# Performance work log

Measured on AMD Instinct MI355X. Metric: run time of the kernel, lower is better.

## Reference

```python
import jax, jax.numpy as jnp
import numpy as np

DIM = 1024
HEADS = 16
BIAS_INIT = 5.0
POST_LOG_SCALE = 1.0


def setup_inputs() -> dict:
    key = jax.random.key(0)
    kx, kw = jax.random.split(key)
    x = jax.random.normal(kx, (2, 2048, DIM), dtype=jnp.float32)
    # nn.Linear(dim, heads): weight [heads, dim], bias initialized to bias_init
    W = jax.random.normal(kw, (HEADS, DIM), dtype=jnp.float32) * (1.0 / np.sqrt(DIM))
    b = jnp.full((HEADS,), BIAS_INIT, dtype=jnp.float32)
    return {"x": x, "W": W, "b": b}


def reference(x, W, b):
    # linear -> [b, n, h], rearrange to [b, h, n], logsigmoid, scale
    logits = jnp.einsum('bnd,hd->bhn', x, W) + b[None, :, None]
    fg = jax.nn.log_sigmoid(logits) * POST_LOG_SCALE
    # cumulative sum over sequence
    fg = jnp.cumsum(fg, axis=-1)
    # pairwise subtract: bias[b,h,i,j] = fg[b,h,i] - fg[b,h,j] (causal case)
    return fg[:, :, :, None] - fg[:, :, None, :]
```

## Files before the change

### kernel.cpp

```cpp
#include <hip/hip_runtime.h>
#include <hip/hip_bf16.h>

#define DIM   1024
#define HEADS 16
#define B     2
#define N     2048
#define RPW   8

typedef float f32x4 __attribute__((ext_vector_type(4)));

__global__ __launch_bounds__(256) void logits_kernel(
    const float* __restrict__ x, const float* __restrict__ W,
    const float* __restrict__ bias, float* __restrict__ logits) {
  const int bn   = blockIdx.x;
  const int tid  = threadIdx.x;
  const int wave = tid >> 6;
  const int lane = tid & 63;

  const f32x4* xrow = (const f32x4*)(x + (size_t)bn * DIM);
  f32x4 xv[4];
#pragma unroll
  for (int k = 0; k < 4; ++k) xv[k] = xrow[lane * 4 + k];

#pragma unroll
  for (int hh = 0; hh < 4; ++hh) {
    const int h = wave * 4 + hh;
    const f32x4* wrow = (const f32x4*)(W + (size_t)h * DIM);
    float s = 0.0f;
#pragma unroll
    for (int k = 0; k < 4; ++k) {
      f32x4 wv = wrow[lane * 4 + k];
      s += wv.x * xv[k].x + wv.y * xv[k].y + wv.z * xv[k].z + wv.w * xv[k].w;
    }
#pragma unroll
    for (int off = 32; off > 0; off >>= 1) s += __shfl_down(s, off, 64);
    if (lane == 0) {
      const int b = bn >> 11;
      const int n = bn & (N - 1);
      logits[((size_t)(b * HEADS + h)) * N + n] = s + bias[h];
    }
  }
}

__device__ __forceinline__ float logsig(float z) {
  return fminf(z, 0.0f) - log1pf(__expf(-fabsf(z)));
}

__global__ __launch_bounds__(256) void cumsum_kernel(
    const float* __restrict__ logits, float* __restrict__ fg) {
  const int bh  = blockIdx.x;
  const int tid = threadIdx.x;
  const float* lp = logits + (size_t)bh * N;
  float*       fp = fg     + (size_t)bh * N;

  f32x4 a = ((const f32x4*)lp)[tid * 2];
  f32x4 c = ((const f32x4*)lp)[tid * 2 + 1];
  float v[8] = {a.x, a.y, a.z, a.w, c.x, c.y, c.z, c.w};

  float run = 0.0f;
#pragma unroll
  for (int i = 0; i < 8; ++i) { v[i] = logsig(v[i]); run += v[i]; v[i] = run; }
  const float total = run;

  const int lane = tid & 63, wv = tid >> 6;
  float sc = total;
#pragma unroll
  for (int off = 1; off < 64; off <<= 1) {
    float t = __shfl_up(sc, off, 64);
    if (lane >= off) sc += t;
  }

  __shared__ float wtot[4];
  if (lane == 63) wtot[wv] = sc;
  __syncthreads();
  float wofs = 0.0f;
  for (int w = 0; w < wv; ++w) wofs += wtot[w];

  const float base = wofs + sc - total;
  f32x4 o0 = {base + v[0], base + v[1], base + v[2], base + v[3]};
  f32x4 o1 = {base + v[4], base + v[5], base + v[6], base + v[7]};
  ((f32x4*)fp)[tid * 2]     = o0;
  ((f32x4*)fp)[tid * 2 + 1] = o1;
}

__global__ __launch_bounds__(256) void outer_kernel(
    const float* __restrict__ fg, float* __restrict__ out) {
  const int tid  = threadIdx.x;
  const int wave = tid >> 6;
  const int lane = tid & 63;
  const int gw   = blockIdx.x * 4 + wave;
  const int row0 = gw * RPW;
  const int bh   = row0 >> 11;
  const int i0   = row0 & (N - 1);

  const float* frow = fg + ((size_t)bh << 11);

  const f32x4* fj = (const f32x4*)frow;
  f32x4 vj[8];
#pragma unroll
  for (int k = 0; k < 8; ++k) vj[k] = fj[lane + k * 64];

  f32x4 fia = *(const f32x4*)(frow + i0);
  f32x4 fib = *(const f32x4*)(frow + i0 + 4);
  const float fi[RPW] = {fia.x, fia.y, fia.z, fia.w, fib.x, fib.y, fib.z, fib.w};

  f32x4* orow = (f32x4*)(out + ((size_t)row0 << 11));
#pragma unroll
  for (int r = 0; r < RPW; ++r) {
    const float f = fi[r];
#pragma unroll
    for (int k = 0; k < 8; ++k) {
      f32x4 v = vj[k];
      f32x4 s = {f - v.x, f - v.y, f - v.z, f - v.w};
      orow[lane + k * 64] = s;
    }
    orow += N / 4;
  }
}

extern "C" void kernel_launch(void* const* d_in, const int* in_sizes, int n_in,
                              void* d_out, int out_size, void* d_ws, size_t ws_size,
                              hipStream_t stream) {
  const float* x    = (const float*)d_in[0];
  const float* W    = (const float*)d_in[1];
  const float* bias = (const float*)d_in[2];
  float* out = (float*)d_out;

  float* logits = (float*)d_ws;
  float* fg     = logits + (size_t)B * HEADS * N;

  logits_kernel<<<B * N, 256, 0, stream>>>(x, W, bias, logits);
  cumsum_kernel<<<B * HEADS, 256, 0, stream>>>(logits, fg);
  outer_kernel<<<B * HEADS * N / (RPW * 4), 256, 0, stream>>>(fg, out);
}
```

Before: 123.4 us.

## Fuse logits, cumsum and outer-difference into one cooperative kernel with grid sync

Merges the three launches into a single cooperative persistent kernel that uses grid-wide syncs between the projection, the scan and the pairwise-difference phases. Each block processes four input rows in the projection phase and each wave writes sixteen output rows in the final phase. This is meant to remove inter-kernel launch gaps and tail effects. It adds grid barrier cost and depends on the grid being co-resident, falling back to separate kernels if the cooperative launch fails.

After: 334.8 us. +171.4%, slower.

```diff
diff --git a/kernel.cpp b/kernel.cpp
--- a/kernel.cpp
+++ b/kernel.cpp
@@ -1,13 +1,127 @@
 #include <hip/hip_runtime.h>
 #include <hip/hip_bf16.h>
+#include <hip/hip_cooperative_groups.h>
+
+namespace cg = cooperative_groups;
 
 #define DIM   1024
 #define HEADS 16
 #define B     2
 #define N     2048
-#define RPW   8
+#define BLOCKS 1024
 
 typedef float f32x4 __attribute__((ext_vector_type(4)));
+
+__device__ __forceinline__ float logsig(float z) {
+  return fminf(z, 0.0f) - log1pf(__expf(-fabsf(z)));
+}
+
+__global__ __launch_bounds__(256, 4) void fused_kernel(
+    const float* __restrict__ x, const float* __restrict__ W,
+    const float* __restrict__ bias, float* __restrict__ out,
+    float* __restrict__ logits, float* __restrict__ fg) {
+  cg::grid_group grid = cg::this_grid();
+  const int tid  = threadIdx.x;
+  const int wave = tid >> 6;
+  const int lane = tid & 63;
+
+  {
+    const int bn0 = blockIdx.x * 4;
+    for (int r = 0; r < 4; ++r) {
+      const int bn = bn0 + r;
+      const f32x4* xrow = (const f32x4*)(x + (size_t)bn * DIM);
+      f32x4 xv[4];
+#pragma unroll
+      for (int k = 0; k < 4; ++k) xv[k] = xrow[lane * 4 + k];
+#pragma unroll
+      for (int hh = 0; hh < 4; ++hh) {
+        const int h = wave * 4 + hh;
+        const f32x4* wrow = (const f32x4*)(W + (size_t)h * DIM);
+        float s = 0.0f;
+#pragma unroll
+        for (int k = 0; k < 4; ++k) {
+          f32x4 wv = wrow[lane * 4 + k];
+          s += wv.x * xv[k].x + wv.y * xv[k].y + wv.z * xv[k].z + wv.w * xv[k].w;
+        }
+#pragma unroll
+        for (int off = 32; off > 0; off >>= 1) s += __shfl_down(s, off, 64);
+        if (lane == 0) {
+          const int b = bn >> 11;
+          const int n = bn & (N - 1);
+          logits[((size_t)(b * HEADS + h)) * N + n] = s + bias[h];
+        }
+      }
+    }
+  }
+
+  grid.sync();
+
+  if (blockIdx.x < B * HEADS) {
+    const int bh = blockIdx.x;
+    const float* lp = logits + (size_t)bh * N;
+    float*       fp = fg     + (size_t)bh * N;
+
+    f32x4 a = ((const f32x4*)lp)[tid * 2];
+    f32x4 c = ((const f32x4*)lp)[tid * 2 + 1];
+    float v[8] = {a.x, a.y, a.z, a.w, c.x, c.y, c.z, c.w};
+
+    float run = 0.0f;
+#pragma unroll
+    for (int i = 0; i < 8; ++i) { v[i] = logsig(v[i]); run += v[i]; v[i] = run; }
+    const float total = run;
+
+    float sc = total;
+#pragma unroll
+    for (int off = 1; off < 64; off <<= 1) {
+      float t = __shfl_up(sc, off, 64);
+      if (lane >= off) sc += t;
+    }
+
+    __shared__ float wtot[4];
+    if (lane == 63) wtot[wave] = sc;
+    __syncthreads();
+    float wofs = 0.0f;
+    for (int w = 0; w < wave; ++w) wofs += wtot[w];
+
+    const float base = wofs + sc - total;
+    f32x4 o0 = {base + v[0], base + v[1], base + v[2], base + v[3]};
+    f32x4 o1 = {base + v[4], base + v[5], base + v[6], base + v[7]};
+    ((f32x4*)fp)[tid * 2]     = o0;
+    ((f32x4*)fp)[tid * 2 + 1] = o1;
+  }
+
+  grid.sync();
+
+  {
+    const int row0 = (blockIdx.x * 4 + wave) * 16;
+    const int bh   = row0 >> 11;
+    const int i0   = row0 & (N - 1);
+    const float* frow = fg + ((size_t)bh << 11);
+
+    const f32x4* fj = (const f32x4*)frow;
+    f32x4 vj[8];
+#pragma unroll
+    for (int k = 0; k < 8; ++k) vj[k] = fj[lane + k * 64];
+
+    f32x4* orow = (f32x4*)(out + ((size_t)row0 << 11));
+#pragma unroll 2
+    for (int q = 0; q < 4; ++q) {
+      f32x4 t = *(const f32x4*)(frow + i0 + 4 * q);
+      const float fi[4] = {t.x, t.y, t.z, t.w};
+#pragma unroll
+      for (int r = 0; r < 4; ++r) {
+        const float f = fi[r];
+#pragma unroll
+        for (int k = 0; k < 8; ++k) {
+          f32x4 v = vj[k];
+          f32x4 s = {f - v.x, f - v.y, f - v.z, f - v.w};
+          orow[lane + k * 64] = s;
+        }
+        orow += N / 4;
+      }
+    }
+  }
+}
 
 __global__ __launch_bounds__(256) void logits_kernel(
     const float* __restrict__ x, const float* __restrict__ W,
@@ -42,10 +156,6 @@
   }
 }
 
-__device__ __forceinline__ float logsig(float z) {
-  return fminf(z, 0.0f) - log1pf(__expf(-fabsf(z)));
-}
-
 __global__ __launch_bounds__(256) void cumsum_kernel(
     const float* __restrict__ logits, float* __restrict__ fg) {
   const int bh  = blockIdx.x;
@@ -85,37 +195,19 @@
 
 __global__ __launch_bounds__(256) void outer_kernel(
     const float* __restrict__ fg, float* __restrict__ out) {
-  const int tid  = threadIdx.x;
-  const int wave = tid >> 6;
-  const int lane = tid & 63;
-  const int gw   = blockIdx.x * 4 + wave;
-  const int row0 = gw * RPW;
-  const int bh   = row0 >> 11;
-  const int i0   = row0 & (N - 1);
-
-  const float* frow = fg + ((size_t)bh << 11);
-
-  const f32x4* fj = (const f32x4*)frow;
-  f32x4 vj[8];
-#pragma unroll
-  for (int k = 0; k < 8; ++k) vj[k] = fj[lane + k * 64];
-
-  f32x4 fia = *(const f32x4*)(frow + i0);
-  f32x4 fib = *(const f32x4*)(frow + i0 + 4);
-  const float fi[RPW] = {fia.x, fia.y, fia.z, fia.w, fib.x, fib.y, fib.z, fib.w};
-
-  f32x4* orow = (f32x4*)(out + ((size_t)row0 << 11));
-#pragma unroll
-  for (int r = 0; r < RPW; ++r) {
-    const float f = fi[r];
-#pragma unroll
-    for (int k = 0; k < 8; ++k) {
-      f32x4 v = vj[k];
-      f32x4 s = {f - v.x, f - v.y, f - v.z, f - v.w};
-      orow[lane + k * 64] = s;
-    }
-    orow += N / 4;
-  }
+  const int row = blockIdx.x;
+  const int bh  = row >> 11;
+  const float fi = fg[(size_t)bh * N + (row & (N - 1))];
+  const f32x4* fj = (const f32x4*)(fg + (size_t)bh * N);
+  f32x4* o = (f32x4*)(out + (size_t)row * N);
+  const int tid = threadIdx.x;
+
+  f32x4 v0 = fj[tid];
+  f32x4 v1 = fj[tid + 256];
+  f32x4 r0 = {fi - v0.x, fi - v0.y, fi - v0.z, fi - v0.w};
+  f32x4 r1 = {fi - v1.x, fi - v1.y, fi - v1.z, fi - v1.w};
+  o[tid]       = r0;
+  o[tid + 256] = r1;
 }
 
 extern "C" void kernel_launch(void* const* d_in, const int* in_sizes, int n_in,
@@ -129,7 +221,14 @@
   float* logits = (float*)d_ws;
   float* fg     = logits + (size_t)B * HEADS * N;
 
-  logits_kernel<<<B * N, 256, 0, stream>>>(x, W, bias, logits);
-  cumsum_kernel<<<B * HEADS, 256, 0, stream>>>(logits, fg);
-  outer_kernel<<<B * HEADS * N / (RPW * 4), 256, 0, stream>>>(fg, out);
-}
+  void* args[] = {(void*)&x, (void*)&W, (void*)&bias,
+                  (void*)&out, (void*)&logits, (void*)&fg};
+  hipError_t err = hipLaunchCooperativeKernel((const void*)fused_kernel,
+                                              dim3(BLOCKS), dim3(256), args, 0,
+                                              stream);
+  if (err != hipSuccess) {
+    logits_kernel<<<B * N, 256, 0, stream>>>(x, W, bias, logits);
+    cumsum_kernel<<<B * HEADS, 256, 0, stream>>>(logits, fg);
+    outer_kernel<<<B * HEADS * N, 256, 0, stream>>>(fg, out);
+  }
+}
```
